# Kernel optimization log

Hardware: AMD Instinct MI355X
Metric: run time of the kernel (lower is better)

## Reference

```python
import jax, jax.numpy as jnp
import numpy as np

B, H, T, K, V, S = 2, 8, 4096, 128, 128, 128
C = T // S


def setup_inputs() -> dict:
    key = jax.random.key(0)
    ks = jax.random.split(key, 5)
    return {
        "q": jax.random.normal(ks[0], (B, H, T, K), jnp.float32),
        "k": jax.random.normal(ks[1], (B, H, T, K), jnp.float32),
        "v": jax.random.normal(ks[2], (B, H, T, V), jnp.float32),
        "i": jax.random.normal(ks[3], (B, H, T), jnp.float32),
        "f": jax.random.normal(ks[4], (B, H, T), jnp.float32),
        "initial_C": jnp.zeros((B, H, K, V), jnp.float32),
        "initial_n": jnp.zeros((B, H, K), jnp.float32),
        "initial_m": jnp.zeros((B, H), jnp.float32),
    }


def _forward(q, k, v, ig, fg, C0, n0, m0):
    scale = 1.0 / np.sqrt(K)
    q = q.reshape(B, H, C, S, K) * scale
    k = k.reshape(B, H, C, S, K)
    v = v.reshape(B, H, C, S, V)
    i = ig.reshape(B, H, C, S)
    lf = jax.nn.log_sigmoid(fg).reshape(B, H, C, S)

    lfacc = jnp.cumsum(lf, axis=3)          # backward gates (intra-chunk cumsum)
    lflast = lfacc[..., -1]                  # (B,H,C) total log-forget per chunk
    # rev_cumsum_off: sum of log_fgates strictly after position t
    fwd_gates_unstab = i + (lflast[..., None] - lfacc)
    m_intra = jnp.max(fwd_gates_unstab, axis=3)          # (B,H,C)
    fgexp = jnp.exp(fwd_gates_unstab - m_intra[..., None])

    kv = jnp.einsum("bhctk,bhctd,bhct->bhckd", k, v, fgexp)
    ksum = jnp.einsum("bhctk,bhct->bhck", k, fgexp)

    # sequential inter-chunk recurrence over C chunks (stabilized)
    def step(carry, xs):
        c, n, m = carry
        kv_j, ks_j, lfl_j, mi_j = xs
        m_new = jnp.maximum(lfl_j + m, mi_j)
        e1 = jnp.exp(lfl_j + m - m_new)   # (B,H)
        e2 = jnp.exp(mi_j - m_new)
        out = (c, n, m)                    # state BEFORE this chunk
        c = c * e1[..., None, None] + kv_j * e2[..., None, None]
        n = n * e1[..., None] + ks_j * e2[..., None]
        return (c, n, m), out

    xs = (jnp.moveaxis(kv, 2, 0), jnp.moveaxis(ksum, 2, 0),
          jnp.moveaxis(lflast, 2, 0), jnp.moveaxis(m_intra, 2, 0))
    _, (c_prev, n_prev, m_prev) = jax.lax.scan(step, (C0, n0, m0), xs)
    c_prev = jnp.moveaxis(c_prev, 0, 2)   # (B,H,C,K,V)
    n_prev = jnp.moveaxis(n_prev, 0, 2)   # (B,H,C,K)
    m_prev = jnp.moveaxis(m_prev, 0, 2)   # (B,H,C)

    # intra-chunk causal forget matrix: G_unstab[s,t] = sum_{u=t+1..s} lf[u] + i[t]
    D = lfacc[..., :, None] - lfacc[..., None, :]        # (B,H,C,S,S)
    mask = jnp.tril(jnp.ones((S, S), bool))
    G_unstab = jnp.where(mask, D + i[:, :, :, None, :], -jnp.inf)
    G_stab = jnp.max(G_unstab, axis=-1)                   # (B,H,C,S)
    G_stab = jnp.maximum(G_stab, m_prev[..., None] + lfacc)
    G = jnp.exp(G_unstab - G_stab[..., None])             # -inf -> 0

    M = jnp.einsum("bhctk,bhcsk,bhcst->bhcst", k, q, G)
    inter_w = jnp.exp(lfacc + m_prev[..., None] - G_stab)  # (B,H,C,S)
    inter_n = jnp.einsum("bhcsk,bhcs,bhck->bhcs", q, inter_w, n_prev)
    M_norm = jnp.maximum(jnp.abs(M.sum(-1) + inter_n), jnp.exp(-G_stab))

    h = jnp.einsum("bhctv,bhcst,bhcs->bhcsv", v, M, 1.0 / M_norm)
    h = h + jnp.einsum("bhckv,bhcsk,bhcs->bhcsv", c_prev, q, inter_w / M_norm)
    return h.reshape(B, H, T, V)


def reference(q, k, v, i, f, initial_C, initial_n, initial_m):
    return _forward(q, k, v, i, f, initial_C, initial_n, initial_m)
```

## Files before the change

kernel.cpp:

```cpp
#include <hip/hip_runtime.h>
#include <hip/hip_fp16.h>
#include <math.h>

#define Bb 2
#define Hh 8
#define Tt 4096
#define Kk 128
#define Vv 128
#define Ss 128
#define Cc 32
#define BH (Bb*Hh)
#define SCALE 0.08838834764831845f

#define OFF_LFACC  0
#define OFF_LFLAST (OFF_LFACC + BH*Tt)
#define OFF_MINTRA (OFF_LFLAST + BH*Cc)
#define OFF_KSUM   (OFF_MINTRA + BH*Cc)
#define OFF_KVH    (OFF_KSUM + BH*Cc*Kk)

typedef _Float16 f16x8 __attribute__((ext_vector_type(8)));
typedef _Float16 f16x4 __attribute__((ext_vector_type(4)));
typedef _Float16 f16x2 __attribute__((ext_vector_type(2)));
typedef float f32x4 __attribute__((ext_vector_type(4)));

union U2 { f16x2 h; unsigned u; };
union U8 { f16x8 v; unsigned u[4]; };

__global__ __launch_bounds__(512, 4) void k_kvg(const float* __restrict__ ig,
                                                const float* __restrict__ fg,
                                                const float* __restrict__ kg,
                                                const float* __restrict__ vg,
                                                float* __restrict__ ws) {
    __shared__ _Float16 Kt[Ss * Ss];
    __shared__ _Float16 Vt[Ss * Ss];
    __shared__ float sfg[Ss];
    __shared__ float scomb[4];

    int blk = blockIdx.x;
    int bh = blk >> 5;
    int c  = blk & 31;
    int tid = threadIdx.x;
    int lane = tid & 63;
    int w = tid >> 6;
    int l15 = lane & 15;
    int g = lane >> 4;

    const float* kb = kg + ((size_t)bh * Tt + (size_t)c * Ss) * Kk;
    const float* vb = vg + ((size_t)bh * Tt + (size_t)c * Ss) * Vv;

    int c0a = (tid & 31) * 4;
    int t0a = (tid >> 5) * 4;
    const float* ksrcA = kb + (size_t)t0a * Kk + c0a;
    const float* vsrcA = vb + (size_t)t0a * Vv + c0a;
    float4 kA0 = *(const float4*)(ksrcA);
    float4 kA1 = *(const float4*)(ksrcA + Kk);
    float4 kA2 = *(const float4*)(ksrcA + 2 * Kk);
    float4 kA3 = *(const float4*)(ksrcA + 3 * Kk);
    float4 vA0 = *(const float4*)(vsrcA);
    float4 vA1 = *(const float4*)(vsrcA + Vv);
    float4 vA2 = *(const float4*)(vsrcA + 2 * Vv);
    float4 vA3 = *(const float4*)(vsrcA + 3 * Vv);
    int tau1 = tid + 512;
    int c0b = (tau1 & 31) * 4;
    int t0b = (tau1 >> 5) * 4;
    const float* ksrcB = kb + (size_t)t0b * Kk + c0b;
    const float* vsrcB = vb + (size_t)t0b * Vv + c0b;
    float4 kB0 = *(const float4*)(ksrcB);
    float4 kB1 = *(const float4*)(ksrcB + Kk);
    float4 kB2 = *(const float4*)(ksrcB + 2 * Kk);
    float4 kB3 = *(const float4*)(ksrcB + 3 * Kk);
    float4 vB0 = *(const float4*)(vsrcB);
    float4 vB1 = *(const float4*)(vsrcB + Vv);
    float4 vB2 = *(const float4*)(vsrcB + 2 * Vv);
    float4 vB3 = *(const float4*)(vsrcB + 3 * Vv);

    bool p0 = tid < Ss;
    int lane64 = tid & 63;
    int wv = (tid >> 6) & 1;
    int gidx = bh * Tt + c * Ss + tid;
    float lfacc = 0.f, fwd = 0.f;
    if (p0) {
        float x  = fg[gidx];
        lfacc = fminf(x, 0.f) - log1pf(__expf(-fabsf(x)));
        for (int off = 1; off < 64; off <<= 1) {
            float o = __shfl_up(lfacc, off);
            if (lane64 >= off) lfacc += o;
        }
        if (lane64 == 63) scomb[wv] = lfacc;
    }
    __syncthreads();
    if (p0) {
        float tot0 = scomb[0];
        if (wv == 1) lfacc += tot0;
        float lflast = tot0 + scomb[1];
        fwd = ig[gidx] + lflast - lfacc;
        float mx = fwd;
        for (int off = 32; off; off >>= 1) mx = fmaxf(mx, __shfl_xor(mx, off));
        if (lane64 == 0) scomb[2 + wv] = mx;
    }
    __syncthreads();
    if (p0) {
        float mi = fmaxf(scomb[2], scomb[3]);
        sfg[tid] = __expf(fwd - mi);
        ws[OFF_LFACC + gidx] = lfacc;
        if (tid == 0) {
            ws[OFF_LFLAST + blk] = scomb[0] + scomb[1];
            ws[OFF_MINTRA + blk] = mi;
        }
    }
    __syncthreads();

    {
        float g0 = sfg[t0a], g1 = sfg[t0a + 1], g2 = sfg[t0a + 2], g3 = sfg[t0a + 3];
#pragma unroll
        for (int jc = 0; jc < 4; jc++) {
            float ke0 = (jc == 0 ? kA0.x : jc == 1 ? kA0.y : jc == 2 ? kA0.z : kA0.w);
            float ke1 = (jc == 0 ? kA1.x : jc == 1 ? kA1.y : jc == 2 ? kA1.z : kA1.w);
            float ke2 = (jc == 0 ? kA2.x : jc == 1 ? kA2.y : jc == 2 ? kA2.z : kA2.w);
            float ke3 = (jc == 0 ? kA3.x : jc == 1 ? kA3.y : jc == 2 ? kA3.z : kA3.w);
            float ve0 = (jc == 0 ? vA0.x : jc == 1 ? vA0.y : jc == 2 ? vA0.z : vA0.w);
            float ve1 = (jc == 0 ? vA1.x : jc == 1 ? vA1.y : jc == 2 ? vA1.z : vA1.w);
            float ve2 = (jc == 0 ? vA2.x : jc == 1 ? vA2.y : jc == 2 ? vA2.z : vA2.w);
            float ve3 = (jc == 0 ? vA3.x : jc == 1 ? vA3.y : jc == 2 ? vA3.z : vA3.w);
            int row = c0a + jc;
            int col = t0a ^ ((row & 15) << 3);
            f16x4 kc = { (_Float16)(ke0 * g0), (_Float16)(ke1 * g1),
                         (_Float16)(ke2 * g2), (_Float16)(ke3 * g3) };
            f16x4 vc = { (_Float16)ve0, (_Float16)ve1, (_Float16)ve2, (_Float16)ve3 };
            *(f16x4*)&Kt[row * Ss + col] = kc;
            *(f16x4*)&Vt[row * Ss + col] = vc;
        }
    }
    {
        float g0 = sfg[t0b], g1 = sfg[t0b + 1], g2 = sfg[t0b + 2], g3 = sfg[t0b + 3];
#pragma unroll
        for (int jc = 0; jc < 4; jc++) {
            float ke0 = (jc == 0 ? kB0.x : jc == 1 ? kB0.y : jc == 2 ? kB0.z : kB0.w);
            float ke1 = (jc == 0 ? kB1.x : jc == 1 ? kB1.y : jc == 2 ? kB1.z : kB1.w);
            float ke2 = (jc == 0 ? kB2.x : jc == 1 ? kB2.y : jc == 2 ? kB2.z : kB2.w);
            float ke3 = (jc == 0 ? kB3.x : jc == 1 ? kB3.y : jc == 2 ? kB3.z : kB3.w);
            float ve0 = (jc == 0 ? vB0.x : jc == 1 ? vB0.y : jc == 2 ? vB0.z : vB0.w);
            float ve1 = (jc == 0 ? vB1.x : jc == 1 ? vB1.y : jc == 2 ? vB1.z : vB1.w);
            float ve2 = (jc == 0 ? vB2.x : jc == 1 ? vB2.y : jc == 2 ? vB2.z : vB2.w);
            float ve3 = (jc == 0 ? vB3.x : jc == 1 ? vB3.y : jc == 2 ? vB3.z : vB3.w);
            int row = c0b + jc;
            int col = t0b ^ ((row & 15) << 3);
            f16x4 kc = { (_Float16)(ke0 * g0), (_Float16)(ke1 * g1),
                         (_Float16)(ke2 * g2), (_Float16)(ke3 * g3) };
            f16x4 vc = { (_Float16)ve0, (_Float16)ve1, (_Float16)ve2, (_Float16)ve3 };
            *(f16x4*)&Kt[row * Ss + col] = kc;
            *(f16x4*)&Vt[row * Ss + col] = vc;
        }
    }
    __syncthreads();

    if (tid < Ss) {
        int sw = (tid & 15) << 3;
        float s = 0.f;
#pragma unroll
        for (int i = 0; i < 16; i++) {
            f16x8 ld = *(const f16x8*)&Kt[tid * Ss + ((8 * i) ^ sw)];
#pragma unroll
            for (int e = 0; e < 8; e++) s += (float)ld[e];
        }
        ws[OFF_KSUM + (size_t)blk * Kk + tid] = s;
    }

    const int band = w * 16;
    const int swt = l15 << 3;
    f16x8 af[4];
#pragma unroll
    for (int kk = 0; kk < 4; kk++)
        af[kk] = *(const f16x8*)&Vt[(band + l15) * Ss + ((kk * 32 + g * 8) ^ swt)];

    f32x4 acc[8];
#pragma unroll
    for (int kj = 0; kj < 8; kj++) acc[kj] = (f32x4){0.f, 0.f, 0.f, 0.f};

#pragma unroll
    for (int kj = 0; kj < 8; kj++) {
        int kr = kj * 16 + l15;
#pragma unroll
        for (int kk = 0; kk < 4; kk++) {
            f16x8 bv = *(const f16x8*)&Kt[kr * Ss + ((kk * 32 + g * 8) ^ swt)];
            acc[kj] = __builtin_amdgcn_mfma_f32_16x16x32_f16(af[kk], bv, acc[kj], 0, 0, 0);
        }
    }

    _Float16* dst = (_Float16*)(ws + OFF_KVH) + (size_t)blk * Kk * Vv;
#pragma unroll
    for (int kj = 0; kj < 8; kj++)
#pragma unroll
        for (int r = 0; r < 4; r++)
            dst[(size_t)(band + 4 * g + r) * Kk + kj * 16 + l15] = (_Float16)acc[kj][r];
}

__global__ __launch_bounds__(128) void k_scan_apply(const float* __restrict__ C0,
                                                    const float* __restrict__ n0,
                                                    const float* __restrict__ m0,
                                                    float* __restrict__ ws) {
    __shared__ float se1[Cc], se2[Cc];
    const int NC2 = BH * Kk * Vv / 2;
    int gid = blockIdx.x * 128 + threadIdx.x;
    bool main_r = gid < NC2;
    int bh = main_r ? (gid >> 13) : ((gid - NC2) >> 7);

    if (threadIdx.x < Cc) {
        int cc = threadIdx.x;
        float m   = m0[bh];
        float lfl = ws[OFF_LFLAST + bh * Cc + cc];
        float mi  = ws[OFF_MINTRA + bh * Cc + cc];
        float mn  = fmaxf(lfl + m, mi);
        se1[cc] = __expf(lfl + m - mn);
        se2[cc] = __expf(mi - mn);
    }
    __syncthreads();

    if (main_r) {
        int i  = gid & 8191;
        int v  = i >> 6;
        int k2 = (i & 63) << 1;
        float st0 = C0[(size_t)bh * Kk * Vv + (size_t)k2 * Vv + v];
        float st1 = C0[(size_t)bh * Kk * Vv + (size_t)(k2 + 1) * Vv + v];
        f16x2* base = (f16x2*)((_Float16*)(ws + OFF_KVH) +
                               (size_t)bh * Cc * Kk * Vv + (size_t)v * Kk + k2);
        const size_t stride = Kk * Vv / 2;
        f16x2 cur = base[0];
        f16x2 nxt = base[stride];
#pragma unroll
        for (int c = 0; c < Cc; c++) {
            f16x2 n2 = (c + 2 < Cc) ? base[(size_t)(c + 2) * stride]
                                    : (f16x2){(_Float16)0.f, (_Float16)0.f};
            f16x2 o = { (_Float16)st0, (_Float16)st1 };
            base[(size_t)c * stride] = o;
            float e1 = se1[c], e2 = se2[c];
            st0 = st0 * e1 + (float)cur[0] * e2;
            st1 = st1 * e1 + (float)cur[1] * e2;
            cur = nxt; nxt = n2;
        }
    } else if (gid < NC2 + BH * Kk) {
        int g2 = gid - NC2;
        float st = n0[g2];
        float* base = ws + OFF_KSUM + (size_t)bh * Cc * Kk + (g2 & (Kk - 1));
        float cur = base[0];
        float nxt = base[Kk];
#pragma unroll
        for (int c = 0; c < Cc; c++) {
            float n2 = (c + 2 < Cc) ? base[(size_t)(c + 2) * Kk] : 0.f;
            float kvv = cur;
            base[(size_t)c * Kk] = st;
            st = st * se1[c] + kvv * se2[c];
            cur = nxt; nxt = n2;
        }
    }
}

__global__ __launch_bounds__(512, 4) void k_out_mfma(const float* __restrict__ qg,
                                                     const float* __restrict__ kg,
                                                     const float* __restrict__ vg,
                                                     const float* __restrict__ ig,
                                                     const float* __restrict__ m0,
                                                     float* __restrict__ ws,
                                                     float* __restrict__ out) {
    __shared__ _Float16 Xb[Ss * Kk];
    __shared__ float sbt[Ss], sas[Ss], siw[Ss], smn[Ss], slfa[Ss], snp[Ss];
    __shared__ float scomb[2];

    int blk = blockIdx.x;
    int bh = blk >> 5;
    int c  = blk & 31;
    int tid = threadIdx.x;
    int lane = tid & 63;
    int w = tid >> 6;
    int l15 = lane & 15;
    int g = lane >> 4;
    const int S0 = w * 16;
    const int swt = l15 << 3;

    const size_t rowbase = (size_t)bh * Tt + (size_t)c * Ss;
    const float* qp = qg + rowbase * Kk;
    const float* kp = kg + rowbase * Kk;
    const float* vp = vg + rowbase * Vv;
    const float* nprev = ws + OFF_KSUM + (size_t)blk * Kk;
    const _Float16* cprevT = (const _Float16*)(ws + OFF_KVH) + (size_t)blk * Kk * Vv;
    const float m_prev = m0[bh];

    {
        int tK  = tid >> 2;
        int khK = (tid & 3) * 32;
        const float* src = kp + (size_t)tK * Kk + khK;
        int sw = (tK & 15) << 3;
#pragma unroll
        for (int i = 0; i < 4; i++) {
            float4 a = *(const float4*)&src[8 * i];
            float4 b = *(const float4*)&src[8 * i + 4];
            f16x8 h;
            h[0]=(_Float16)a.x; h[1]=(_Float16)a.y; h[2]=(_Float16)a.z; h[3]=(_Float16)a.w;
            h[4]=(_Float16)b.x; h[5]=(_Float16)b.y; h[6]=(_Float16)b.z; h[7]=(_Float16)b.w;
            int col = (khK + 8 * i) ^ sw;
            *(f16x8*)&Xb[tK * Kk + col] = h;
        }
    }

    f16x8 qf[4];
#pragma unroll
    for (int kk = 0; kk < 4; kk++) {
        const float* p = qp + (size_t)(S0 + l15) * Kk + kk * 32 + g * 8;
        float4 a = *(const float4*)p;
        float4 b = *(const float4*)(p + 4);
        f16x8 r;
        r[0]=(_Float16)a.x; r[1]=(_Float16)a.y; r[2]=(_Float16)a.z; r[3]=(_Float16)a.w;
        r[4]=(_Float16)b.x; r[5]=(_Float16)b.y; r[6]=(_Float16)b.z; r[7]=(_Float16)b.w;
        qf[kk] = r;
    }

    bool p0 = tid < Ss;
    int lane64 = tid & 63;
    int wv = (tid >> 6) & 1;
    float pm = 0.f;
    if (p0) {
        float lfa = ws[OFF_LFACC + bh * Tt + c * Ss + tid];
        float bt = ig[bh * Tt + c * Ss + tid] - lfa;
        sbt[tid] = bt;
        slfa[tid] = lfa;
        snp[tid] = nprev[tid];
        pm = bt;
        for (int off = 1; off < 64; off <<= 1) {
            float o = __shfl_up(pm, off);
            if (lane64 >= off) pm = fmaxf(pm, o);
        }
        if (lane64 == 63) scomb[wv] = pm;
    }
    __syncthreads();

    const int t0A = w * 8;
    const int t0B = (8 + w) * 8;
    float vra[8], vrb[8], vrc[8], vrd[8];
#pragma unroll
    for (int i = 0; i < 8; i++) {
        vra[i] = vp[(size_t)(t0A + i) * Vv + lane];
        vrb[i] = vp[(size_t)(t0A + i) * Vv + lane + 64];
        vrc[i] = vp[(size_t)(t0B + i) * Vv + lane];
        vrd[i] = vp[(size_t)(t0B + i) * Vv + lane + 64];
    }

    if (p0) {
        if (wv == 1) pm = fmaxf(pm, scomb[0]);
        float mx = fmaxf(pm, m_prev);
        sas[tid] = -mx;
        siw[tid] = SCALE * __expf(m_prev - mx);
    }
    float dotq = 0.f;
#pragma unroll
    for (int kk = 0; kk < 4; kk++)
#pragma unroll
        for (int e = 0; e < 8; e++)
            dotq += (float)qf[kk][e] * snp[kk * 32 + g * 8 + e];
    dotq += __shfl_xor(dotq, 16);
    dotq += __shfl_xor(dotq, 32);

    f16x8 hva, hvb, hvc, hvd;
#pragma unroll
    for (int i = 0; i < 8; i++) {
        hva[i] = (_Float16)vra[i];  hvb[i] = (_Float16)vrb[i];
        hvc[i] = (_Float16)vrc[i];  hvd[i] = (_Float16)vrd[i];
    }
    __syncthreads();

    const float as_s = sas[S0 + l15];
    const float iw_s = siw[S0 + l15];
    const float lfa_s = slfa[S0 + l15];

    unsigned plo[8] = {0,0,0,0,0,0,0,0};
    unsigned phi[8] = {0,0,0,0,0,0,0,0};
    float rs = 0.f;
#pragma unroll
    for (int tj = 0; tj < 8; tj++) {
        if (tj <= w) {
            int trow = tj * 16 + l15;
            f16x8 bfr[4];
#pragma unroll
            for (int kk = 0; kk < 4; kk++)
                bfr[kk] = *(const f16x8*)&Xb[trow * Kk + ((kk * 32 + g * 8) ^ swt)];
            f32x4 acc = {0.f, 0.f, 0.f, 0.f};
#pragma unroll
            for (int kk = 0; kk < 4; kk++)
                acc = __builtin_amdgcn_mfma_f32_16x16x32_f16(bfr[kk], qf[kk], acc, 0, 0, 0);
            float vals[4];
#pragma unroll
            for (int r = 0; r < 4; r++) {
                int t = tj * 16 + 4 * g + r;
                float btv = sbt[t];
                float val = acc[r] * SCALE * __expf(as_s + btv);
                if (tj == w && (4 * g + r) > l15) val = 0.f;
                rs += val;
                vals[r] = val;
            }
            U2 lo, hi;
            lo.h = (f16x2){ (_Float16)vals[0], (_Float16)vals[1] };
            hi.h = (f16x2){ (_Float16)vals[2], (_Float16)vals[3] };
            plo[tj] = lo.u;
            phi[tj] = hi.u;
        }
    }
    rs += __shfl_xor(rs, 16);
    rs += __shfl_xor(rs, 32);
    {
        float engs = __expf(as_s - lfa_s);
        float mn = fmaxf(fabsf(rs + dotq * iw_s), engs);
        if (g == 0) smn[S0 + l15] = mn;
    }
    __syncthreads();

    {
        int sw = (lane & 15) << 3;
        *(f16x8*)&Xb[lane * Ss + (t0A ^ sw)] = hva;
        *(f16x8*)&Xb[(lane + 64) * Ss + (t0A ^ sw)] = hvb;
        *(f16x8*)&Xb[lane * Ss + (t0B ^ sw)] = hvc;
        *(f16x8*)&Xb[(lane + 64) * Ss + (t0B ^ sw)] = hvd;
    }

    f16x8 pb[4];
    const int kmax = w >> 1;
    {
        int a2 = (g & 1) * 2;
        int sA = a2 * 16 + l15;
        int sB = sA + 16;
        bool hi2 = (g >> 1) != 0;
#pragma unroll
        for (int kkt = 0; kkt < 4; kkt++) {
            if (kkt <= kmax) {
                unsigned xA0 = __shfl((int)plo[2*kkt],   sA);
                unsigned xA1 = __shfl((int)phi[2*kkt],   sA);
                unsigned xB0 = __shfl((int)plo[2*kkt],   sB);
                unsigned xB1 = __shfl((int)phi[2*kkt],   sB);
                unsigned yA0 = __shfl((int)plo[2*kkt+1], sA);
                unsigned yA1 = __shfl((int)phi[2*kkt+1], sA);
                unsigned yB0 = __shfl((int)plo[2*kkt+1], sB);
                unsigned yB1 = __shfl((int)phi[2*kkt+1], sB);
                U8 t;
                t.u[0] = hi2 ? yA0 : xA0;
                t.u[1] = hi2 ? yA1 : xA1;
                t.u[2] = hi2 ? yB0 : xB0;
                t.u[3] = hi2 ? yB1 : xB1;
                pb[kkt] = t.v;
            }
        }
    }
    __syncthreads();

    const float rnv_s = 1.0f / smn[S0 + l15];

#pragma unroll
    for (int half = 0; half < 2; half++) {
        f32x4 h4[4];
#pragma unroll
        for (int j = 0; j < 4; j++) h4[j] = (f32x4){0.f, 0.f, 0.f, 0.f};

#pragma unroll
        for (int kkt = 0; kkt < 4; kkt++) {
            if (kkt <= kmax) {
#pragma unroll
                for (int j = 0; j < 4; j++) {
                    int vr = (half * 4 + j) * 16 + l15;
                    f16x8 av = *(const f16x8*)&Xb[vr * Ss + ((kkt * 32 + g * 8) ^ swt)];
                    h4[j] = __builtin_amdgcn_mfma_f32_16x16x32_f16(av, pb[kkt], h4[j], 0, 0, 0);
                }
            }
        }
#pragma unroll
        for (int j = 0; j < 4; j++) {
            int vr = (half * 4 + j) * 16 + l15;
            f32x4 tmp = {0.f, 0.f, 0.f, 0.f};
            const _Float16* cpr = cprevT + (size_t)vr * Kk + g * 8;
#pragma unroll
            for (int kk = 0; kk < 4; kk++) {
                f16x8 bcf = *(const f16x8*)(cpr + kk * 32);
                tmp = __builtin_amdgcn_mfma_f32_16x16x32_f16(bcf, qf[kk], tmp, 0, 0, 0);
            }
            float4 o;
            o.x = (h4[j][0] + tmp[0] * iw_s) * rnv_s;
            o.y = (h4[j][1] + tmp[1] * iw_s) * rnv_s;
            o.z = (h4[j][2] + tmp[2] * iw_s) * rnv_s;
            o.w = (h4[j][3] + tmp[3] * iw_s) * rnv_s;
            *(float4*)&out[(rowbase + S0 + l15) * Vv + (half * 4 + j) * 16 + 4 * g] = o;
        }
    }
}

extern "C" void kernel_launch(void* const* d_in, const int* in_sizes, int n_in,
                              void* d_out, int out_size, void* d_ws, size_t ws_size,
                              hipStream_t stream) {
    (void)in_sizes; (void)n_in; (void)out_size; (void)ws_size;
    const float* q  = (const float*)d_in[0];
    const float* k  = (const float*)d_in[1];
    const float* v  = (const float*)d_in[2];
    const float* ig = (const float*)d_in[3];
    const float* fg = (const float*)d_in[4];
    const float* C0 = (const float*)d_in[5];
    const float* n0 = (const float*)d_in[6];
    const float* m0 = (const float*)d_in[7];
    float* out = (float*)d_out;
    float* ws  = (float*)d_ws;

    k_kvg<<<BH * Cc, 512, 0, stream>>>(ig, fg, k, v, ws);
    k_scan_apply<<<(BH * Kk * Vv / 2 + BH * Kk) / 128, 128, 0, stream>>>(C0, n0, m0, ws);
    k_out_mfma<<<BH * Cc, 512, 0, stream>>>(q, k, v, ig, m0, ws, out);
}
```

Before: 63.23 us.

## Stage fp16 swizzled K/V images in workspace and load via global_load_lds

```diff
diff --git a/kernel.cpp b/kernel.cpp
--- a/kernel.cpp
+++ b/kernel.cpp
@@ -17,6 +17,8 @@
 #define OFF_MINTRA (OFF_LFLAST + BH*Cc)
 #define OFF_KSUM   (OFF_MINTRA + BH*Cc)
 #define OFF_KVH    (OFF_KSUM + BH*Cc*Kk)
+#define OFF_KIMG   (OFF_KVH + BH*Cc*Kk*Vv/2)
+#define OFF_VIMG   (OFF_KIMG + BH*Tt*Kk/2)
 
 typedef _Float16 f16x8 __attribute__((ext_vector_type(8)));
 typedef _Float16 f16x4 __attribute__((ext_vector_type(4)));
@@ -25,6 +27,10 @@
 
 union U2 { f16x2 h; unsigned u; };
 union U8 { f16x8 v; unsigned u[4]; };
+
+#define GLDS16(gp, lp) __builtin_amdgcn_global_load_lds( \
+    (const __attribute__((address_space(1))) void*)(gp), \
+    (__attribute__((address_space(3))) void*)(lp), 16, 0, 0)
 
 __global__ __launch_bounds__(512, 4) void k_kvg(const float* __restrict__ ig,
                                                 const float* __restrict__ fg,
@@ -47,6 +53,8 @@
 
     const float* kb = kg + ((size_t)bh * Tt + (size_t)c * Ss) * Kk;
     const float* vb = vg + ((size_t)bh * Tt + (size_t)c * Ss) * Vv;
+    _Float16* kimgw = (_Float16*)(ws + OFF_KIMG) + (size_t)blk * Ss * Kk;
+    _Float16* vimgw = (_Float16*)(ws + OFF_VIMG) + (size_t)blk * Ss * Kk;
 
     int c0a = (tid & 31) * 4;
     int t0a = (tid >> 5) * 4;
@@ -110,6 +118,23 @@
     }
     __syncthreads();
 
+#pragma unroll
+    for (int jr = 0; jr < 4; jr++) {
+        float4 kr4 = (jr == 0 ? kA0 : jr == 1 ? kA1 : jr == 2 ? kA2 : kA3);
+        int t = t0a + jr;
+        int col = c0a ^ ((t & 15) << 3);
+        f16x4 h = { (_Float16)kr4.x, (_Float16)kr4.y, (_Float16)kr4.z, (_Float16)kr4.w };
+        *(f16x4*)&kimgw[(size_t)t * Kk + col] = h;
+    }
+#pragma unroll
+    for (int jr = 0; jr < 4; jr++) {
+        float4 kr4 = (jr == 0 ? kB0 : jr == 1 ? kB1 : jr == 2 ? kB2 : kB3);
+        int t = t0b + jr;
+        int col = c0b ^ ((t & 15) << 3);
+        f16x4 h = { (_Float16)kr4.x, (_Float16)kr4.y, (_Float16)kr4.z, (_Float16)kr4.w };
+        *(f16x4*)&kimgw[(size_t)t * Kk + col] = h;
+    }
+
     {
         float g0 = sfg[t0a], g1 = sfg[t0a + 1], g2 = sfg[t0a + 2], g3 = sfg[t0a + 3];
 #pragma unroll
@@ -154,6 +179,11 @@
     }
     __syncthreads();
 
+#pragma unroll
+    for (int p = 0; p < 4; p++)
+        *(f16x8*)&vimgw[(size_t)(p * 512 + tid) * 8] =
+            *(const f16x8*)&Vt[(p * 512 + tid) * 8];
+
     if (tid < Ss) {
         int sw = (tid & 15) << 3;
         float s = 0.f;
@@ -256,14 +286,13 @@
 }
 
 __global__ __launch_bounds__(512, 4) void k_out_mfma(const float* __restrict__ qg,
-                                                     const float* __restrict__ kg,
-                                                     const float* __restrict__ vg,
                                                      const float* __restrict__ ig,
                                                      const float* __restrict__ m0,
                                                      float* __restrict__ ws,
                                                      float* __restrict__ out) {
-    __shared__ _Float16 Xb[Ss * Kk];
-    __shared__ float sbt[Ss], sas[Ss], siw[Ss], smn[Ss], slfa[Ss], snp[Ss];
+    __shared__ _Float16 XbK[Ss * Kk];
+    __shared__ _Float16 XbV[Ss * Kk];
+    __shared__ float sbt[Ss], sas[Ss], siw[Ss], slfa[Ss], snp[Ss];
     __shared__ float scomb[2];
 
     int blk = blockIdx.x;
@@ -279,27 +308,17 @@
 
     const size_t rowbase = (size_t)bh * Tt + (size_t)c * Ss;
     const float* qp = qg + rowbase * Kk;
-    const float* kp = kg + rowbase * Kk;
-    const float* vp = vg + rowbase * Vv;
     const float* nprev = ws + OFF_KSUM + (size_t)blk * Kk;
     const _Float16* cprevT = (const _Float16*)(ws + OFF_KVH) + (size_t)blk * Kk * Vv;
+    const _Float16* kimg = (const _Float16*)(ws + OFF_KIMG) + (size_t)blk * Ss * Kk;
+    const _Float16* vimg = (const _Float16*)(ws + OFF_VIMG) + (size_t)blk * Ss * Kk;
     const float m_prev = m0[bh];
 
-    {
-        int tK  = tid >> 2;
-        int khK = (tid & 3) * 32;
-        const float* src = kp + (size_t)tK * Kk + khK;
-        int sw = (tK & 15) << 3;
-#pragma unroll
-        for (int i = 0; i < 4; i++) {
-            float4 a = *(const float4*)&src[8 * i];
-            float4 b = *(const float4*)&src[8 * i + 4];
-            f16x8 h;
-            h[0]=(_Float16)a.x; h[1]=(_Float16)a.y; h[2]=(_Float16)a.z; h[3]=(_Float16)a.w;
-            h[4]=(_Float16)b.x; h[5]=(_Float16)b.y; h[6]=(_Float16)b.z; h[7]=(_Float16)b.w;
-            int col = (khK + 8 * i) ^ sw;
-            *(f16x8*)&Xb[tK * Kk + col] = h;
-        }
+#pragma unroll
+    for (int p = 0; p < 4; p++) {
+        int unit = p * 512 + w * 64;
+        GLDS16(kimg + (size_t)(unit + lane) * 8, &XbK[unit * 8]);
+        GLDS16(vimg + (size_t)(unit + lane) * 8, &XbV[unit * 8]);
     }
 
     f16x8 qf[4];
@@ -333,17 +352,6 @@
     }
     __syncthreads();
 
-    const int t0A = w * 8;
-    const int t0B = (8 + w) * 8;
-    float vra[8], vrb[8], vrc[8], vrd[8];
-#pragma unroll
-    for (int i = 0; i < 8; i++) {
-        vra[i] = vp[(size_t)(t0A + i) * Vv + lane];
-        vrb[i] = vp[(size_t)(t0A + i) * Vv + lane + 64];
-        vrc[i] = vp[(size_t)(t0B + i) * Vv + lane];
-        vrd[i] = vp[(size_t)(t0B + i) * Vv + lane + 64];
-    }
-
     if (p0) {
         if (wv == 1) pm = fmaxf(pm, scomb[0]);
         float mx = fmaxf(pm, m_prev);
@@ -358,13 +366,6 @@
             dotq += (float)qf[kk][e] * snp[kk * 32 + g * 8 + e];
     dotq += __shfl_xor(dotq, 16);
     dotq += __shfl_xor(dotq, 32);
-
-    f16x8 hva, hvb, hvc, hvd;
-#pragma unroll
-    for (int i = 0; i < 8; i++) {
-        hva[i] = (_Float16)vra[i];  hvb[i] = (_Float16)vrb[i];
-        hvc[i] = (_Float16)vrc[i];  hvd[i] = (_Float16)vrd[i];
-    }
     __syncthreads();
 
     const float as_s = sas[S0 + l15];
@@ -381,7 +382,7 @@
             f16x8 bfr[4];
 #pragma unroll
             for (int kk = 0; kk < 4; kk++)
-                bfr[kk] = *(const f16x8*)&Xb[trow * Kk + ((kk * 32 + g * 8) ^ swt)];
+                bfr[kk] = *(const f16x8*)&XbK[trow * Kk + ((kk * 32 + g * 8) ^ swt)];
             f32x4 acc = {0.f, 0.f, 0.f, 0.f};
 #pragma unroll
             for (int kk = 0; kk < 4; kk++)
@@ -405,20 +406,8 @@
     }
     rs += __shfl_xor(rs, 16);
     rs += __shfl_xor(rs, 32);
-    {
-        float engs = __expf(as_s - lfa_s);
-        float mn = fmaxf(fabsf(rs + dotq * iw_s), engs);
-        if (g == 0) smn[S0 + l15] = mn;
-    }
-    __syncthreads();
-
-    {
-        int sw = (lane & 15) << 3;
-        *(f16x8*)&Xb[lane * Ss + (t0A ^ sw)] = hva;
-        *(f16x8*)&Xb[(lane + 64) * Ss + (t0A ^ sw)] = hvb;
-        *(f16x8*)&Xb[lane * Ss + (t0B ^ sw)] = hvc;
-        *(f16x8*)&Xb[(lane + 64) * Ss + (t0B ^ sw)] = hvd;
-    }
+    float engs = __expf(as_s - lfa_s);
+    float rnv_s = 1.0f / fmaxf(fabsf(rs + dotq * iw_s), engs);
 
     f16x8 pb[4];
     const int kmax = w >> 1;
@@ -447,9 +436,6 @@
             }
         }
     }
-    __syncthreads();
-
-    const float rnv_s = 1.0f / smn[S0 + l15];
 
 #pragma unroll
     for (int half = 0; half < 2; half++) {
@@ -463,7 +449,7 @@
 #pragma unroll
                 for (int j = 0; j < 4; j++) {
                     int vr = (half * 4 + j) * 16 + l15;
-                    f16x8 av = *(const f16x8*)&Xb[vr * Ss + ((kkt * 32 + g * 8) ^ swt)];
+                    f16x8 av = *(const f16x8*)&XbV[vr * Ss + ((kkt * 32 + g * 8) ^ swt)];
                     h4[j] = __builtin_amdgcn_mfma_f32_16x16x32_f16(av, pb[kkt], h4[j], 0, 0, 0);
                 }
             }
@@ -505,5 +491,5 @@
 
     k_kvg<<<BH * Cc, 512, 0, stream>>>(ig, fg, k, v, ws);
     k_scan_apply<<<(BH * Kk * Vv / 2 + BH * Kk) / 128, 128, 0, stream>>>(C0, n0, m0, ws);
-    k_out_mfma<<<BH * Cc, 512, 0, stream>>>(q, k, v, ig, m0, ws, out);
+    k_out_mfma<<<BH * Cc, 512, 0, stream>>>(q, ig, m0, ws, out);
 }
```

Result: faster. 60.67 us (-4.0%).
